# Kernel optimization log

Hardware: AMD Instinct MI355X
Metric: run time of the kernel (lower is better)

Reference implementation:

```python
import jax, jax.numpy as jnp
import numpy as np

EPS = 1e-3        # Sinkhorn regularization (SinkhornDistance default)
MAX_ITER = 10     # max Sinkhorn iterations
THRESH = 0.1      # early-stop threshold on |u - u_prev|
N, P, D = 8, 2048, 64


def _l2norm(x):
    # F.normalize(x, dim=-1): x / max(||x||_2, 1e-12)
    return x / jnp.maximum(jnp.linalg.norm(x, axis=-1, keepdims=True), 1e-12)


def _l1norm(x):
    # F.normalize(x, p=1, dim=-1)
    return x / jnp.maximum(jnp.sum(jnp.abs(x), axis=-1, keepdims=True), 1e-12)


def _M(C, u, v):
    # modified cost M_ij = (-C_ij + u_i + v_j) / eps
    return (-C + u[..., :, None] + v[..., None, :]) / EPS


def _sinkhorn_uv(C, mu, nu):
    """Log-domain Sinkhorn with early stopping (matches torch loop + err.item() break)."""
    u0 = jnp.zeros_like(mu)
    v0 = jnp.zeros_like(nu)

    def cond(st):
        i, u, v, err = st
        return jnp.logical_and(i < MAX_ITER, err >= THRESH)

    def body(st):
        i, u, v, _ = st
        u1 = u
        u = EPS * (jnp.log(mu + 1e-8) - jax.nn.logsumexp(_M(C, u, v), axis=-1)) + u
        # logsumexp of M^T over last dim == logsumexp of M over axis -2
        v = EPS * (jnp.log(nu + 1e-8) - jax.nn.logsumexp(_M(C, u, v), axis=-2)) + v
        err = jnp.mean(jnp.sum(jnp.abs(u - u1), axis=-1))
        return (i + 1, u, v, err)

    _, u, v, _ = jax.lax.while_loop(
        cond, body, (jnp.int32(0), u0, v0, jnp.float32(jnp.inf)))
    return u, v


def setup_inputs() -> dict:
    key = jax.random.key(0)
    ka, kb = jax.random.split(key)
    a = jax.random.normal(ka, (N, P, D), dtype=jnp.float32)
    b = jax.random.normal(kb, (N, P, D), dtype=jnp.float32)
    return {"a": a, "b": b}


def reference(a, b):
    a = _l2norm(a)
    b = _l2norm(b)
    cost = 1.0 - jnp.einsum('bnd,bmd->bnm', a, b)          # [N, P1, P2]

    # weights computed from detached cost
    Cd = jax.lax.stop_gradient(cost)
    S = 1.0 - Cd
    wa = _l1norm(jnp.clip(_l1norm(jnp.mean(S, axis=2)), 0.0))  # [N, P1]
    wb = _l1norm(jnp.clip(_l1norm(jnp.mean(S, axis=1)), 0.0))  # [N, P2]

    u, v = _sinkhorn_uv(Cd, wa, wb)
    pi = jax.lax.stop_gradient(jnp.exp(_M(Cd, u, v)))       # transport plan, detached
    D_out = jnp.sum(pi * cost, axis=(-2, -1))               # [N], reduction='none'
    return D_out
```

## Files before the change

kernel.cpp:

```cpp
#include <hip/hip_runtime.h>
#include <math.h>

#define NB 8
#define PP 2048
#define DD 64
#define EPSF 1e-3f
#define RCPE 1000.0f
#define TMAX 10
#define THRESHF 0.1f
#define NEG_INF (-1e30f)
#define QSCALE 32767.5f
#define S_DEQ  (1.0f / 32767.5f)
#define KR 512
#define KC 512
#define TSEL 0.15f

typedef __attribute__((ext_vector_type(8))) short bf16x8;
typedef __attribute__((ext_vector_type(4))) float f32x4;

__device__ __forceinline__ float waveAllMax(float v) {
#pragma unroll
    for (int m = 1; m < 64; m <<= 1) v = fmaxf(v, __shfl_xor(v, m, 64));
    return v;
}
__device__ __forceinline__ float waveAllMin(float v) {
#pragma unroll
    for (int m = 1; m < 64; m <<= 1) v = fminf(v, __shfl_xor(v, m, 64));
    return v;
}
__device__ __forceinline__ float waveAllSum(float v) {
#pragma unroll
    for (int m = 1; m < 64; m <<= 1) v += __shfl_xor(v, m, 64);
    return v;
}
__device__ __forceinline__ short f2bf(float x) {
    unsigned b = __float_as_uint(x);
    return (short)((b + 0x7FFFu + ((b >> 16) & 1u)) >> 16);
}
__device__ __forceinline__ float bf2f(short h) {
    return __uint_as_float(((unsigned)(unsigned short)h) << 16);
}

__global__ void norm_kernel(const float* __restrict__ a, const float* __restrict__ b,
                            short* __restrict__ ahi, short* __restrict__ alo,
                            short* __restrict__ bhi, short* __restrict__ blo,
                            float* __restrict__ u, float* __restrict__ v,
                            int* __restrict__ conv, float* __restrict__ out,
                            float* __restrict__ Sa) {
    int gt = blockIdx.x * 256 + threadIdx.x;
    if (gt < NB * PP) { u[gt] = 0.0f; v[gt] = 0.0f; }
    if (gt == 0) *conv = 0;
    if (gt < NB) out[gt] = 0.0f;
    if (gt < 2 * NB * DD) Sa[gt] = 0.0f;
    int wave = gt >> 6;
    int lane = threadIdx.x & 63;
    const float* src; short* dhi; short* dlo; int row;
    if (wave < NB * PP) { src = a; dhi = ahi; dlo = alo; row = wave; }
    else                { src = b; dhi = bhi; dlo = blo; row = wave - NB * PP; }
    float x = src[(size_t)row * DD + lane];
    float ss = waveAllSum(x * x);
    float r = 1.0f / fmaxf(sqrtf(ss), 1e-12f);
    float xn = x * r;
    short h = f2bf(xn);
    dhi[(size_t)row * DD + lane] = h;
    dlo[(size_t)row * DD + lane] = f2bf(xn - bf2f(h));
}

__global__ void sumvec_kernel(const short* __restrict__ ahi, const short* __restrict__ alo,
                              const short* __restrict__ bhi, const short* __restrict__ blo,
                              float* __restrict__ Sa, float* __restrict__ Sb) {
    int b = blockIdx.x >> 3;
    bool isB = (blockIdx.x >> 2) & 1;
    int qtr = blockIdx.x & 3;
    const short* hi = (isB ? bhi : ahi) + ((size_t)b * PP + qtr * 512) * DD;
    const short* lo = (isB ? blo : alo) + ((size_t)b * PP + qtr * 512) * DD;
    float* dst = (isB ? Sb : Sa) + b * DD;
    int t = threadIdx.x;
    int w = t >> 6, lane = t & 63;
    int rl = lane >> 3, dq = lane & 7;
    float s[8] = {};
#pragma unroll
    for (int it = 0; it < 16; ++it) {
        size_t o = (size_t)(w * 128 + it * 8 + rl) * DD + dq * 8;
        bf16x8 h = *(const bf16x8*)(hi + o);
        bf16x8 l = *(const bf16x8*)(lo + o);
#pragma unroll
        for (int e = 0; e < 8; ++e) s[e] += bf2f(h[e]) + bf2f(l[e]);
    }
#pragma unroll
    for (int e = 0; e < 8; ++e) {
#pragma unroll
        for (int m = 8; m < 64; m <<= 1) s[e] += __shfl_xor(s[e], m, 64);
    }
    __shared__ float sh[4][64];
    if (rl == 0) {
#pragma unroll
        for (int e = 0; e < 8; ++e) sh[w][dq * 8 + e] = s[e];
    }
    __syncthreads();
    if (t < 64) atomicAdd(&dst[t], sh[0][t] + sh[1][t] + sh[2][t] + sh[3][t]);
}

__global__ __launch_bounds__(256) void cost_kernel(const short* __restrict__ ahi,
        const short* __restrict__ alo, const short* __restrict__ bhi,
        const short* __restrict__ blo, unsigned short* __restrict__ C16,
        unsigned* __restrict__ rminp, unsigned* __restrict__ cminp) {
    __shared__ unsigned cmin2[4][64];
    int b  = blockIdx.z;
    int i0 = blockIdx.y * 128;
    int j0 = blockIdx.x * 64;
    int t = threadIdx.x, w = t >> 6, lane = t & 63;
    int quad = lane >> 4, li = lane & 15;
    size_t Aoff = ((size_t)b * PP + i0 + w * 32) * DD;
    size_t Boff = ((size_t)b * PP + j0) * DD;
    f32x4 acc[2][4] = {};
#pragma unroll
    for (int kc = 0; kc < 2; ++kc) {
        int k0 = kc * 32 + quad * 8;
        bf16x8 fah[2], fal[2];
#pragma unroll
        for (int mt = 0; mt < 2; ++mt) {
            size_t o = Aoff + (size_t)(mt * 16 + li) * DD + k0;
            fah[mt] = *(const bf16x8*)(ahi + o);
            fal[mt] = *(const bf16x8*)(alo + o);
        }
#pragma unroll
        for (int nt = 0; nt < 4; ++nt) {
            size_t o = Boff + (size_t)(li * 4 + nt) * DD + k0;
            bf16x8 fbh = *(const bf16x8*)(bhi + o);
            bf16x8 fbl = *(const bf16x8*)(blo + o);
#pragma unroll
            for (int mt = 0; mt < 2; ++mt) {
                acc[mt][nt] = __builtin_amdgcn_mfma_f32_16x16x32_bf16(
                        fah[mt], fbh, acc[mt][nt], 0, 0, 0);
                acc[mt][nt] = __builtin_amdgcn_mfma_f32_16x16x32_bf16(
                        fah[mt], fbl, acc[mt][nt], 0, 0, 0);
                acc[mt][nt] = __builtin_amdgcn_mfma_f32_16x16x32_bf16(
                        fal[mt], fbh, acc[mt][nt], 0, 0, 0);
            }
        }
    }
    unsigned cmin[4] = {0xFFFFFFFFu, 0xFFFFFFFFu, 0xFFFFFFFFu, 0xFFFFFFFFu};
#pragma unroll
    for (int mt = 0; mt < 2; ++mt) {
#pragma unroll
        for (int r = 0; r < 4; ++r) {
            int irow = w * 32 + mt * 16 + quad * 4 + r;
            unsigned rm = 0xFFFFFFFFu;
            unsigned short qv[4];
#pragma unroll
            for (int nt = 0; nt < 4; ++nt) {
                float dot = acc[mt][nt][r];
                float cost = fminf(fmaxf(1.0f - dot, 0.0f), 2.0f);
                unsigned q = __float2uint_rn(cost * QSCALE);
                qv[nt] = (unsigned short)q;
                rm = min(rm, (q << 16) | (unsigned)(j0 + li * 4 + nt));
                cmin[nt] = min(cmin[nt], (q << 16) | (unsigned)(i0 + irow));
            }
            *(ushort4*)&C16[((size_t)b * PP + i0 + irow) * PP + j0 + li * 4] =
                make_ushort4(qv[0], qv[1], qv[2], qv[3]);
#pragma unroll
            for (int m = 1; m < 16; m <<= 1)
                rm = min(rm, (unsigned)__shfl_xor((int)rm, m, 64));
            if (li == 0)
                rminp[(size_t)blockIdx.x * (NB * PP) + b * PP + i0 + irow] = rm;
        }
    }
#pragma unroll
    for (int nt = 0; nt < 4; ++nt) {
        unsigned cmv = cmin[nt];
        cmv = min(cmv, (unsigned)__shfl_xor((int)cmv, 16, 64));
        cmv = min(cmv, (unsigned)__shfl_xor((int)cmv, 32, 64));
        if (quad == 0) cmin2[w][li * 4 + nt] = cmv;
    }
    __syncthreads();
    if (t < 64)
        cminp[(size_t)blockIdx.y * (NB * PP) + b * PP + j0 + t] =
            min(min(cmin2[0][t], cmin2[1][t]), min(cmin2[2][t], cmin2[3][t]));
}

__global__ void combine_kernel(const unsigned* __restrict__ rminp,
                               const unsigned* __restrict__ cminp,
                               unsigned* __restrict__ rowminp, unsigned* __restrict__ colminp) {
    int idx = blockIdx.x * 256 + threadIdx.x;
    unsigned rm = 0xFFFFFFFFu, cm = 0xFFFFFFFFu;
#pragma unroll
    for (int k = 0; k < 32; ++k)
        rm = min(rm, rminp[(size_t)k * (NB * PP) + idx]);
#pragma unroll
    for (int k = 0; k < 16; ++k)
        cm = min(cm, cminp[(size_t)k * (NB * PP) + idx]);
    rowminp[idx] = rm; colminp[idx] = cm;
}

__device__ __forceinline__ float blockReduceSum256(float v, float* sh) {
    v = waveAllSum(v);
    int lane = threadIdx.x & 63, w = threadIdx.x >> 6;
    if (lane == 0) sh[w] = v;
    __syncthreads();
    float r = sh[0] + sh[1] + sh[2] + sh[3];
    __syncthreads();
    return r;
}

__global__ void weights_kernel(const float* __restrict__ Sa, const float* __restrict__ Sb,
                               const short* __restrict__ ahi, const short* __restrict__ alo,
                               const short* __restrict__ bhi, const short* __restrict__ blo,
                               const unsigned* __restrict__ rowminp, const unsigned* __restrict__ colminp,
                               float* __restrict__ elm, float* __restrict__ eln,
                               float* __restrict__ rowminf, float* __restrict__ colminf,
                               float* __restrict__ cthresh) {
    __shared__ float sh[4];
    __shared__ float sv[64];
    int b = blockIdx.x & 7;
    bool isB = blockIdx.x >= 8;
    const short* hi = (isB ? bhi : ahi) + (size_t)b * PP * DD;
    const short* lo = (isB ? blo : alo) + (size_t)b * PP * DD;
    const float* svecg = (isB ? Sa : Sb) + b * DD;
    float* dst = (isB ? eln : elm) + b * PP;
    int tid = threadIdx.x;
    if (tid < 64) sv[tid] = svecg[tid];
    __syncthreads();
    float x[8];
    float sabs = 0.0f;
#pragma unroll
    for (int q = 0; q < 8; ++q) {
        int row = tid + q * 256;
        float dot = 0.0f;
#pragma unroll
        for (int dq = 0; dq < 8; ++dq) {
            bf16x8 h = *(const bf16x8*)(hi + (size_t)row * DD + dq * 8);
            bf16x8 l = *(const bf16x8*)(lo + (size_t)row * DD + dq * 8);
#pragma unroll
            for (int e = 0; e < 8; ++e)
                dot += (bf2f(h[e]) + bf2f(l[e])) * sv[dq * 8 + e];
        }
        x[q] = dot * (1.0f / (float)PP);
        sabs += fabsf(x[q]);
    }
    sabs = blockReduceSum256(sabs, sh);
    float inv1 = 1.0f / fmaxf(sabs, 1e-12f);
    float spos = 0.0f;
#pragma unroll
    for (int q = 0; q < 8; ++q) {
        x[q] = fmaxf(x[q] * inv1, 0.0f);
        spos += x[q];
    }
    spos = blockReduceSum256(spos, sh);
    float inv2 = 1.0f / fmaxf(spos, 1e-12f);
#pragma unroll
    for (int q = 0; q < 8; ++q)
        dst[tid + q * 256] = EPSF * logf(x[q] * inv2 + 1e-8f);
    if (isB) {
#pragma unroll
        for (int q = 0; q < 8; ++q) {
            int idx = b * PP + tid + q * 256;
            unsigned pc = colminp[idx];
            unsigned arg = pc & 0xffffu;
            unsigned pr = rowminp[b * PP + arg];
            float cmf = (float)(pc >> 16) * S_DEQ;
            colminf[idx] = cmf;
            cthresh[idx] = cmf - (float)(pr >> 16) * S_DEQ + TSEL;
        }
    } else {
#pragma unroll
        for (int q = 0; q < 8; ++q) {
            int idx = b * PP + tid + q * 256;
            rowminf[idx] = (float)(rowminp[idx] >> 16) * S_DEQ;
        }
    }
}

__global__ __launch_bounds__(256) void select_kernel(const unsigned short* __restrict__ C16,
        const float* __restrict__ colminf, const float* __restrict__ rowminf,
        const float* __restrict__ cthresh,
        unsigned* __restrict__ rlist, int* __restrict__ rcnt,
        unsigned* __restrict__ clist, int* __restrict__ scnt) {
    __shared__ unsigned tile32[64][36];
    __shared__ float rm_s[64];
    __shared__ unsigned lcnt[64];
    if (blockIdx.x < 4096) {
        int w = threadIdx.x >> 6, lane = threadIdx.x & 63;
        int row = blockIdx.x * 4 + w;
        int b = row >> 11;
        const uint4* cp = (const uint4*)(C16 + (size_t)row * PP);
        uint4 q4[4];
#pragma unroll
        for (int g = 0; g < 4; ++g) q4[g] = cp[g * 64 + lane];
        const float* cmb = colminf + b * PP;
        float rpmin = 1e30f;
#pragma unroll
        for (int g = 0; g < 4; ++g) {
            int jb = g * 512 + lane * 8;
            float4 cm0 = *(const float4*)(cmb + jb);
            float4 cm1 = *(const float4*)(cmb + jb + 4);
            float cm[8] = {cm0.x, cm0.y, cm0.z, cm0.w, cm1.x, cm1.y, cm1.z, cm1.w};
            unsigned qq[4] = {q4[g].x, q4[g].y, q4[g].z, q4[g].w};
#pragma unroll
            for (int h = 0; h < 4; ++h) {
                float c0 = (float)(qq[h] & 0xffffu) * S_DEQ;
                float c1 = (float)(qq[h] >> 16) * S_DEQ;
                rpmin = fminf(rpmin, fminf(c0 - cm[h * 2], c1 - cm[h * 2 + 1]));
            }
        }
        float rth = waveAllMin(rpmin) + TSEL;
        int base = 0;
#pragma unroll
        for (int g = 0; g < 4; ++g) {
            int jb = g * 512 + lane * 8;
            float4 cm0 = *(const float4*)(cmb + jb);
            float4 cm1 = *(const float4*)(cmb + jb + 4);
            float cm[8] = {cm0.x, cm0.y, cm0.z, cm0.w, cm1.x, cm1.y, cm1.z, cm1.w};
            unsigned qq[4] = {q4[g].x, q4[g].y, q4[g].z, q4[g].w};
#pragma unroll
            for (int e = 0; e < 8; ++e) {
                unsigned q = (qq[e >> 1] >> ((e & 1) * 16)) & 0xffffu;
                float cf = (float)q * S_DEQ;
                bool rq = (cf - cm[e]) <= rth;
                unsigned long long mb = __ballot(rq);
                if (rq) {
                    int pos = base + __popcll(mb & ((1ull << lane) - 1ull));
                    if (pos < KR) rlist[(size_t)row * KR + pos] = ((unsigned)(jb + e) << 16) | q;
                }
                base += __popcll(mb);
            }
        }
        if (lane == 0) rcnt[row] = base;
    } else {
        int bid = blockIdx.x - 4096;
        int b = bid >> 7;
        int rem = bid & 127;
        int j0 = (rem >> 2) * 64;
        int r0 = (rem & 3) * 512;
        int qq = rem & 3;
        int t = threadIdx.x;
        int col = t & 63, seg = t >> 6;
        float ctj = cthresh[b * PP + j0 + col];
        unsigned* mylist = clist + ((size_t)(b * PP + j0 + col)) * KC + qq * 128;
        if (t < 64) lcnt[t] = 0;
        int lrow = t >> 3, lcc = t & 7;
        uint4 pf0, pf1; float pfr = 0.0f;
        {
            const unsigned short* base0 = C16 + ((size_t)b * PP + r0 + lrow) * PP + j0;
            pf0 = ((const uint4*)base0)[lcc];
            pf1 = ((const uint4*)(base0 + (size_t)32 * PP))[lcc];
            if (t < 64) pfr = rowminf[b * PP + r0 + t];
        }
        for (int chunk = 0; chunk < 8; ++chunk) {
            *(uint4*)&tile32[lrow][lcc * 4]      = pf0;
            *(uint4*)&tile32[32 + lrow][lcc * 4] = pf1;
            if (t < 64) rm_s[t] = pfr;
            __syncthreads();
            if (chunk < 7) {
                int rn = r0 + (chunk + 1) * 64;
                const unsigned short* base0 = C16 + ((size_t)b * PP + rn + lrow) * PP + j0;
                pf0 = ((const uint4*)base0)[lcc];
                pf1 = ((const uint4*)(base0 + (size_t)32 * PP))[lcc];
                if (t < 64) pfr = rowminf[b * PP + rn + t];
            }
            int rbase = r0 + chunk * 64;
#pragma unroll
            for (int rr = 0; rr < 16; ++rr) {
                int row = seg * 16 + rr;
                unsigned w32 = tile32[row][col >> 1];
                unsigned q = (col & 1) ? (w32 >> 16) : (w32 & 0xffffu);
                float cf = (float)q * S_DEQ;
                if (cf - rm_s[row] <= ctj) {
                    unsigned pos = atomicAdd(&lcnt[col], 1u);
                    if (pos < 128) mylist[pos] = ((unsigned)(rbase + row) << 16) | q;
                }
            }
            __syncthreads();
        }
        if (t < 64)
            scnt[(b * PP + j0 + t) * 4 + qq] = min((int)lcnt[t], 128);
    }
}

__global__ __launch_bounds__(256) void u_kernel(const unsigned* __restrict__ rlist,
        const int* __restrict__ rcnt, const float* __restrict__ v,
        const float* __restrict__ elm, float* __restrict__ u, float* __restrict__ du,
        const int* __restrict__ conv) {
    if (*conv) return;
    int w = threadIdx.x >> 6, lane = threadIdx.x & 63;
    int row = blockIdx.x * 4 + w;
    int b = row >> 11;
    int cnt = min(rcnt[row], KR);
    const unsigned* lst = rlist + (size_t)row * KR;
    const float* vb = v + (b << 11);
    float x[8];
    float m = NEG_INF;
#pragma unroll
    for (int s = 0; s < 8; ++s) {
        int e = lane + s * 64;
        x[s] = NEG_INF;
        if (e < cnt) {
            unsigned wd = lst[e];
            x[s] = vb[wd >> 16] - (float)(wd & 0xffffu) * S_DEQ;
        }
        m = fmaxf(m, x[s]);
    }
    m = waveAllMax(m);
    float s = 0.0f;
#pragma unroll
    for (int k = 0; k < 8; ++k) s += __expf((x[k] - m) * RCPE);
    s = waveAllSum(s);
    if (lane == 0) {
        float un = elm[row] - m - EPSF * logf(s);
        du[row] = fabsf(un - u[row]);
        u[row] = un;
    }
}

__global__ __launch_bounds__(256) void v_kernel(const unsigned* __restrict__ clist,
        const int* __restrict__ scnt, const float* __restrict__ u,
        const float* __restrict__ eln, float* __restrict__ v,
        const float* __restrict__ du, int* __restrict__ conv) {
    if (*conv) return;
    int w = threadIdx.x >> 6, lane = threadIdx.x & 63;
    int jg = blockIdx.x * 4 + w;
    int b = jg >> 11;
    int4 sc = *(const int4*)&scnt[jg * 4];
    int cn[4] = {sc.x, sc.y, sc.z, sc.w};
    const unsigned* lst = clist + (size_t)jg * KC;
    const float* ub = u + (b << 11);
    float x[8];
    float m = NEG_INF;
#pragma unroll
    for (int s = 0; s < 8; ++s) {
        int e = lane + s * 64;
        int sg = e >> 7, k = e & 127;
        x[s] = NEG_INF;
        if (k < cn[sg]) {
            unsigned wd = lst[sg * 128 + k];
            x[s] = ub[wd >> 16] - (float)(wd & 0xffffu) * S_DEQ;
        }
        m = fmaxf(m, x[s]);
    }
    m = waveAllMax(m);
    float s = 0.0f;
#pragma unroll
    for (int k = 0; k < 8; ++k) s += __expf((x[k] - m) * RCPE);
    s = waveAllSum(s);
    if (lane == 0)
        v[jg] = eln[jg] - m - EPSF * logf(s);
    if (blockIdx.x == 0) {
        __shared__ float sh[4];
        int t = threadIdx.x;
        float sacc = 0.0f;
#pragma unroll
        for (int q = 0; q < 64; ++q) sacc += du[t + q * 256];
        sacc = waveAllSum(sacc);
        if (lane == 0) sh[w] = sacc;
        __syncthreads();
        if (t == 0) {
            float tot = sh[0] + sh[1] + sh[2] + sh[3];
            if (tot * (1.0f / (float)NB) < THRESHF) *conv = 1;
        }
    }
}

__global__ __launch_bounds__(256) void emd_kernel(const unsigned* __restrict__ rlist,
        const int* __restrict__ rcnt, const float* __restrict__ u,
        const float* __restrict__ v, float* __restrict__ epart) {
    __shared__ float sh[4];
    int w = threadIdx.x >> 6, lane = threadIdx.x & 63;
    int row = blockIdx.x * 4 + w;
    int b = row >> 11;
    int cnt = min(rcnt[row], KR);
    const unsigned* lst = rlist + (size_t)row * KR;
    const float* vb = v + (b << 11);
    float ui = u[row];
    float s = 0.0f;
#pragma unroll
    for (int k = 0; k < 8; ++k) {
        int e = lane + k * 64;
        if (e < cnt) {
            unsigned wd = lst[e];
            float cf = (float)(wd & 0xffffu) * S_DEQ;
            s += __expf((ui + vb[wd >> 16] - cf) * RCPE) * cf;
        }
    }
    s = waveAllSum(s);
    if (lane == 0) sh[w] = s;
    __syncthreads();
    if (threadIdx.x == 0) epart[blockIdx.x] = sh[0] + sh[1] + sh[2] + sh[3];
}

__global__ __launch_bounds__(256) void emd_finalize(const float* __restrict__ epart,
                                                    float* __restrict__ out) {
    __shared__ float sh[4];
    int b = blockIdx.x;
    int t = threadIdx.x;
    float s = epart[b * 512 + t] + epart[b * 512 + 256 + t];
    s = blockReduceSum256(s, sh);
    if (t == 0) out[b] = s;
}

extern "C" void kernel_launch(void* const* d_in, const int* in_sizes, int n_in,
                              void* d_out, int out_size, void* d_ws, size_t ws_size,
                              hipStream_t stream) {
    const float* a = (const float*)d_in[0];
    const float* b = (const float*)d_in[1];
    float* out = (float*)d_out;

    const size_t MBs = 1024ull * 1024ull;
    char* ws = (char*)d_ws;
    unsigned short* C16 = (unsigned short*)ws;
    short* ahi   = (short*)(ws + 64 * MBs);
    short* alo   = (short*)(ws + 66 * MBs);
    short* bhi   = (short*)(ws + 68 * MBs);
    short* blo   = (short*)(ws + 70 * MBs);
    unsigned* rminp = (unsigned*)(ws + 72 * MBs);
    unsigned* cminp = (unsigned*)(ws + 74 * MBs);
    unsigned* rlist = (unsigned*)(ws + 64 * MBs);
    unsigned* clist = (unsigned*)(ws + 96 * MBs);
    char* tail = ws + 128 * MBs;
    size_t off = 0;
    const size_t szV = (size_t)NB * PP * 4;
    int*   scnt    = (int*)(tail + off); off += (size_t)NB * PP * 4 * 4;
    unsigned* rowminp = (unsigned*)(tail + off); off += szV;
    unsigned* colminp = (unsigned*)(tail + off); off += szV;
    float* rowminf = (float*)(tail + off); off += szV;
    float* colminf = (float*)(tail + off); off += szV;
    float* cthresh = (float*)(tail + off); off += szV;
    float* elm     = (float*)(tail + off); off += szV;
    float* eln     = (float*)(tail + off); off += szV;
    float* u       = (float*)(tail + off); off += szV;
    float* v       = (float*)(tail + off); off += szV;
    float* du      = (float*)(tail + off); off += szV;
    int*   rcnt    = (int*)(tail + off); off += szV;
    float* Sa      = (float*)(tail + off); off += (size_t)2 * NB * DD * 4;
    float* Sb      = Sa + NB * DD;
    float* epart   = (float*)(tail + off); off += (size_t)NB * PP / 4 * 4;
    int*   conv    = (int*)(tail + off); off += 64;
    if (ws_size < 128 * MBs + off) return;

    norm_kernel<<<(2 * NB * PP) / 4, 256, 0, stream>>>(a, b, ahi, alo, bhi, blo,
            u, v, conv, out, Sa);
    sumvec_kernel<<<64, 256, 0, stream>>>(ahi, alo, bhi, blo, Sa, Sb);
    cost_kernel<<<dim3(PP / 64, PP / 128, NB), 256, 0, stream>>>(
            ahi, alo, bhi, blo, C16, rminp, cminp);
    combine_kernel<<<64, 256, 0, stream>>>(rminp, cminp, rowminp, colminp);
    weights_kernel<<<16, 256, 0, stream>>>(Sa, Sb, ahi, alo, bhi, blo,
            rowminp, colminp, elm, eln, rowminf, colminf, cthresh);
    select_kernel<<<4096 + 1024, 256, 0, stream>>>(C16, colminf, rowminf,
            cthresh, rlist, rcnt, clist, scnt);
    for (int it = 0; it < TMAX; ++it) {
        u_kernel<<<NB * PP / 4, 256, 0, stream>>>(rlist, rcnt, v, elm, u, du, conv);
        v_kernel<<<NB * PP / 4, 256, 0, stream>>>(clist, scnt, u, eln, v, du, conv);
    }
    emd_kernel<<<NB * PP / 4, 256, 0, stream>>>(rlist, rcnt, u, v, epart);
    emd_finalize<<<NB, 256, 0, stream>>>(epart, out);
}
```

Before: 362.6 us.

## Widen cost tile to 128 columns with swizzled LDS staging of B operands

The cost kernel now computes 128x128 tiles instead of 128x64. It stages the B hi/lo fragments into LDS with an XOR swizzle so all four waves reuse them instead of each wave reading them from global memory. Quantization now uses a packed v_cvt_pknorm_u16 on (1-dot)/2, and the row/column min-key reduction and combine loop are adjusted for half as many column blocks. This adds 32KB of LDS per block and one barrier, which may limit occupancy. The packed conversion changes rounding slightly compared with the old clamp-and-scale path.

```diff
diff --git a/kernel.cpp b/kernel.cpp
--- a/kernel.cpp
+++ b/kernel.cpp
@@ -39,6 +39,11 @@
 }
 __device__ __forceinline__ float bf2f(short h) {
     return __uint_as_float(((unsigned)(unsigned short)h) << 16);
+}
+__device__ __forceinline__ unsigned pknorm_u16(float a, float b) {
+    unsigned r;
+    asm("v_cvt_pknorm_u16_f32 %0, %1, %2" : "=v"(r) : "v"(a), "v"(b));
+    return r;
 }
 
 __global__ void norm_kernel(const float* __restrict__ a, const float* __restrict__ b,
@@ -101,19 +106,36 @@
     if (t < 64) atomicAdd(&dst[t], sh[0][t] + sh[1][t] + sh[2][t] + sh[3][t]);
 }
 
-__global__ __launch_bounds__(256) void cost_kernel(const short* __restrict__ ahi,
+__global__ __launch_bounds__(256, 4) void cost_kernel(const short* __restrict__ ahi,
         const short* __restrict__ alo, const short* __restrict__ bhi,
         const short* __restrict__ blo, unsigned short* __restrict__ C16,
         unsigned* __restrict__ rminp, unsigned* __restrict__ cminp) {
-    __shared__ unsigned cmin2[4][64];
+    __shared__ short Bs[2][128 * 64];
+    __shared__ unsigned cmin2[4][128];
     int b  = blockIdx.z;
     int i0 = blockIdx.y * 128;
-    int j0 = blockIdx.x * 64;
+    int j0 = blockIdx.x * 128;
     int t = threadIdx.x, w = t >> 6, lane = t & 63;
     int quad = lane >> 4, li = lane & 15;
+    const char* bh = (const char*)(bhi + ((size_t)b * PP + j0) * DD);
+    const char* bl = (const char*)(blo + ((size_t)b * PP + j0) * DD);
+    uint4 st[8];
+#pragma unroll
+    for (int i = 0; i < 4; ++i) {
+        unsigned x = (unsigned)(t + i * 256) * 16;
+        unsigned sx = x ^ (((x >> 7) & 7u) << 4);
+        st[i]     = *(const uint4*)(bh + sx);
+        st[4 + i] = *(const uint4*)(bl + sx);
+    }
+#pragma unroll
+    for (int i = 0; i < 4; ++i) {
+        unsigned x = (unsigned)(t + i * 256) * 16;
+        *(uint4*)((char*)&Bs[0][0] + x) = st[i];
+        *(uint4*)((char*)&Bs[1][0] + x) = st[4 + i];
+    }
+    __syncthreads();
     size_t Aoff = ((size_t)b * PP + i0 + w * 32) * DD;
-    size_t Boff = ((size_t)b * PP + j0) * DD;
-    f32x4 acc[2][4] = {};
+    f32x4 acc[2][2][4] = {};
 #pragma unroll
     for (int kc = 0; kc < 2; ++kc) {
         int k0 = kc * 32 + quad * 8;
@@ -125,40 +147,55 @@
             fal[mt] = *(const bf16x8*)(alo + o);
         }
 #pragma unroll
-        for (int nt = 0; nt < 4; ++nt) {
-            size_t o = Boff + (size_t)(li * 4 + nt) * DD + k0;
-            bf16x8 fbh = *(const bf16x8*)(bhi + o);
-            bf16x8 fbl = *(const bf16x8*)(blo + o);
-#pragma unroll
-            for (int mt = 0; mt < 2; ++mt) {
-                acc[mt][nt] = __builtin_amdgcn_mfma_f32_16x16x32_bf16(
-                        fah[mt], fbh, acc[mt][nt], 0, 0, 0);
-                acc[mt][nt] = __builtin_amdgcn_mfma_f32_16x16x32_bf16(
-                        fah[mt], fbl, acc[mt][nt], 0, 0, 0);
-                acc[mt][nt] = __builtin_amdgcn_mfma_f32_16x16x32_bf16(
-                        fal[mt], fbh, acc[mt][nt], 0, 0, 0);
+        for (int nh = 0; nh < 2; ++nh) {
+#pragma unroll
+            for (int ntl = 0; ntl < 4; ++ntl) {
+                int col = nh * 64 + li * 4 + ntl;
+                unsigned xo = ((unsigned)col * 128 + (unsigned)(kc * 4 + quad) * 16)
+                              ^ (((unsigned)col & 7u) << 4);
+                bf16x8 fbh = *(const bf16x8*)((const char*)&Bs[0][0] + xo);
+                bf16x8 fbl = *(const bf16x8*)((const char*)&Bs[1][0] + xo);
+#pragma unroll
+                for (int mt = 0; mt < 2; ++mt) {
+                    acc[mt][nh][ntl] = __builtin_amdgcn_mfma_f32_16x16x32_bf16(
+                            fah[mt], fbh, acc[mt][nh][ntl], 0, 0, 0);
+                    acc[mt][nh][ntl] = __builtin_amdgcn_mfma_f32_16x16x32_bf16(
+                            fah[mt], fbl, acc[mt][nh][ntl], 0, 0, 0);
+                    acc[mt][nh][ntl] = __builtin_amdgcn_mfma_f32_16x16x32_bf16(
+                            fal[mt], fbh, acc[mt][nh][ntl], 0, 0, 0);
+                }
             }
         }
     }
-    unsigned cmin[4] = {0xFFFFFFFFu, 0xFFFFFFFFu, 0xFFFFFFFFu, 0xFFFFFFFFu};
+    unsigned cmin[2][4] = {{0xFFFFFFFFu, 0xFFFFFFFFu, 0xFFFFFFFFu, 0xFFFFFFFFu},
+                           {0xFFFFFFFFu, 0xFFFFFFFFu, 0xFFFFFFFFu, 0xFFFFFFFFu}};
 #pragma unroll
     for (int mt = 0; mt < 2; ++mt) {
 #pragma unroll
         for (int r = 0; r < 4; ++r) {
             int irow = w * 32 + mt * 16 + quad * 4 + r;
             unsigned rm = 0xFFFFFFFFu;
-            unsigned short qv[4];
-#pragma unroll
-            for (int nt = 0; nt < 4; ++nt) {
-                float dot = acc[mt][nt][r];
-                float cost = fminf(fmaxf(1.0f - dot, 0.0f), 2.0f);
-                unsigned q = __float2uint_rn(cost * QSCALE);
-                qv[nt] = (unsigned short)q;
-                rm = min(rm, (q << 16) | (unsigned)(j0 + li * 4 + nt));
-                cmin[nt] = min(cmin[nt], (q << 16) | (unsigned)(i0 + irow));
+            unsigned rowkey = (unsigned)(i0 + irow);
+#pragma unroll
+            for (int nh = 0; nh < 2; ++nh) {
+                float f0 = fmaf(acc[mt][nh][0][r], -0.5f, 0.5f);
+                float f1 = fmaf(acc[mt][nh][1][r], -0.5f, 0.5f);
+                float f2 = fmaf(acc[mt][nh][2][r], -0.5f, 0.5f);
+                float f3 = fmaf(acc[mt][nh][3][r], -0.5f, 0.5f);
+                unsigned w0 = pknorm_u16(f0, f1);
+                unsigned w1 = pknorm_u16(f2, f3);
+                uint2 pv; pv.x = w0; pv.y = w1;
+                *(uint2*)&C16[((size_t)b * PP + i0 + irow) * PP + j0 + nh * 64 + li * 4] = pv;
+                unsigned colb = (unsigned)(j0 + nh * 64 + li * 4);
+                unsigned lo0 = w0 << 16, hi0 = w0 & 0xFFFF0000u;
+                unsigned lo1 = w1 << 16, hi1 = w1 & 0xFFFF0000u;
+                rm = min(rm, min(min(lo0 | colb, hi0 | (colb + 1)),
+                                 min(lo1 | (colb + 2), hi1 | (colb + 3))));
+                cmin[nh][0] = min(cmin[nh][0], lo0 | rowkey);
+                cmin[nh][1] = min(cmin[nh][1], hi0 | rowkey);
+                cmin[nh][2] = min(cmin[nh][2], lo1 | rowkey);
+                cmin[nh][3] = min(cmin[nh][3], hi1 | rowkey);
             }
-            *(ushort4*)&C16[((size_t)b * PP + i0 + irow) * PP + j0 + li * 4] =
-                make_ushort4(qv[0], qv[1], qv[2], qv[3]);
 #pragma unroll
             for (int m = 1; m < 16; m <<= 1)
                 rm = min(rm, (unsigned)__shfl_xor((int)rm, m, 64));
@@ -167,14 +204,17 @@
         }
     }
 #pragma unroll
-    for (int nt = 0; nt < 4; ++nt) {
-        unsigned cmv = cmin[nt];
-        cmv = min(cmv, (unsigned)__shfl_xor((int)cmv, 16, 64));
-        cmv = min(cmv, (unsigned)__shfl_xor((int)cmv, 32, 64));
-        if (quad == 0) cmin2[w][li * 4 + nt] = cmv;
-    }
-    __syncthreads();
-    if (t < 64)
+    for (int nh = 0; nh < 2; ++nh) {
+#pragma unroll
+        for (int ntl = 0; ntl < 4; ++ntl) {
+            unsigned cmv = cmin[nh][ntl];
+            cmv = min(cmv, (unsigned)__shfl_xor((int)cmv, 16, 64));
+            cmv = min(cmv, (unsigned)__shfl_xor((int)cmv, 32, 64));
+            if (quad == 0) cmin2[w][nh * 64 + li * 4 + ntl] = cmv;
+        }
+    }
+    __syncthreads();
+    if (t < 128)
         cminp[(size_t)blockIdx.y * (NB * PP) + b * PP + j0 + t] =
             min(min(cmin2[0][t], cmin2[1][t]), min(cmin2[2][t], cmin2[3][t]));
 }
@@ -185,7 +225,7 @@
     int idx = blockIdx.x * 256 + threadIdx.x;
     unsigned rm = 0xFFFFFFFFu, cm = 0xFFFFFFFFu;
 #pragma unroll
-    for (int k = 0; k < 32; ++k)
+    for (int k = 0; k < 16; ++k)
         rm = min(rm, rminp[(size_t)k * (NB * PP) + idx]);
 #pragma unroll
     for (int k = 0; k < 16; ++k)
@@ -539,7 +579,7 @@
     norm_kernel<<<(2 * NB * PP) / 4, 256, 0, stream>>>(a, b, ahi, alo, bhi, blo,
             u, v, conv, out, Sa);
     sumvec_kernel<<<64, 256, 0, stream>>>(ahi, alo, bhi, blo, Sa, Sb);
-    cost_kernel<<<dim3(PP / 64, PP / 128, NB), 256, 0, stream>>>(
+    cost_kernel<<<dim3(PP / 128, PP / 128, NB), 256, 0, stream>>>(
             ahi, alo, bhi, blo, C16, rminp, cminp);
     combine_kernel<<<64, 256, 0, stream>>>(rminp, cminp, rowminp, colminp);
     weights_kernel<<<16, 256, 0, stream>>>(Sa, Sb, ahi, alo, bhi, blo,
```

Measured after the change: 335.6 us. 1.08x faster.
